# Kernel optimization log

Measured on AMD Instinct MI355X. Metric: run time of the kernel, lower is better.

The kernel has to match this reference:

```python
import jax, jax.numpy as jnp
import numpy as np

DIM = 128
N_NODES = 100000
N_EDGES = 640000


def setup_inputs() -> dict:
    key = jax.random.key(0)
    k1, k2, k3, k4, k5, k6 = jax.random.split(key, 6)
    x = jax.random.normal(k1, (N_NODES, DIM), dtype=jnp.float32)
    edge_index = jax.random.randint(k2, (2, N_EDGES), 0, N_NODES, dtype=jnp.int64)
    edge_weight = jax.random.uniform(k3, (N_EDGES,), dtype=jnp.float32)
    # Linear(dim, dim) params (PyTorch stores weight as [out, in])
    bound = 1.0 / np.sqrt(DIM)
    W = jax.random.uniform(k4, (DIM, DIM), minval=-bound, maxval=bound, dtype=jnp.float32)
    b = jax.random.uniform(k5, (DIM,), minval=-bound, maxval=bound, dtype=jnp.float32)
    alpha = jnp.float32(0.5)
    return {"x": x, "edge_index": edge_index, "num_nodes": N_NODES,
            "edge_weight": edge_weight, "W": W, "b": b, "alpha": alpha}


def reference(x, edge_index, num_nodes, edge_weight, W, b, alpha):
    src = edge_index[0]
    dst = edge_index[1]
    msg = x[src] * edge_weight[:, None]                      # [E, D] gather + weight
    agg = jax.ops.segment_sum(msg, dst, num_segments=num_nodes)   # [N, D] scatter-add
    deg = jax.ops.segment_sum(jnp.ones_like(edge_weight), dst, num_segments=num_nodes)
    deg = jnp.maximum(deg, 1.0)                              # clamp(min=1.0)
    agg = agg / deg[:, None]                                 # mean normalization
    return x + alpha * (agg @ W.T + b)                       # linear + alpha residual
```

## Files before the change

### kernel.cpp

```cpp
#include <hip/hip_runtime.h>
#include <hip/hip_bf16.h>

#define DIM 128
#define NPB 512
#define NPB_SHIFT 9

#define A1_EPT 8
#define A1_EPB (256 * A1_EPT)
#define NBLK_STRIDE 512

#define FROWS 64
#define FPAD 136

typedef __attribute__((ext_vector_type(8))) short bf16x8;
typedef __attribute__((ext_vector_type(8))) unsigned short u16x8;
typedef __attribute__((ext_vector_type(4))) float f32x4;

__device__ __forceinline__ short f2bf(float f) {
    union { __hip_bfloat16 h; short s; } u;
    u.h = __float2bfloat16(f);
    return u.s;
}
__device__ __forceinline__ float bf2f(unsigned short s) {
    union { unsigned int u; float f; } c;
    c.u = ((unsigned int)s) << 16;
    return c.f;
}

__device__ __forceinline__ int load_dst(const void* eidx, int flag64, int E, int e) {
    return flag64 ? (int)((const long long*)eidx)[E + e] : ((const int*)eidx)[E + e];
}
__device__ __forceinline__ int load_src(const void* eidx, int flag64, int E, int e) {
    return flag64 ? (int)((const long long*)eidx)[e] : ((const int*)eidx)[e];
}

__global__ __launch_bounds__(256) void prep_kernel(
        const float* __restrict__ x, unsigned short* __restrict__ xb, int n8,
        const unsigned int* __restrict__ e, int* __restrict__ flags) {
    const int stride = gridDim.x * blockDim.x;
    const int t0 = blockIdx.x * blockDim.x + threadIdx.x;
    for (int t = t0; t < n8; t += stride) {
        const float4* pp = (const float4*)(x + (size_t)t * 8);
        float4 a = pp[0], b = pp[1];
        u16x8 o;
        o[0] = (unsigned short)f2bf(a.x); o[1] = (unsigned short)f2bf(a.y);
        o[2] = (unsigned short)f2bf(a.z); o[3] = (unsigned short)f2bf(a.w);
        o[4] = (unsigned short)f2bf(b.x); o[5] = (unsigned short)f2bf(b.y);
        o[6] = (unsigned short)f2bf(b.z); o[7] = (unsigned short)f2bf(b.w);
        *(u16x8*)(xb + (size_t)t * 8) = o;
    }
    if (blockIdx.x == 0 && threadIdx.x == 0) {
        int ok64 = 1;
        for (int t = 0; t < 128; ++t) {
            if (e[2 * t + 1] != 0u) { ok64 = 0; break; }
        }
        flags[0] = ok64;
    }
}

__global__ __launch_bounds__(256) void part1_kernel(
        const void* __restrict__ eidx, int* __restrict__ bhistT,
        const int* __restrict__ flags, int E) {
    __shared__ int bcnt[256];
    const int tid = threadIdx.x;
    const int blk = blockIdx.x;
    const int base = blk * A1_EPB;
    const int f = flags[0];
    bcnt[tid] = 0;
    __syncthreads();
    #pragma unroll
    for (int i = 0; i < A1_EPT; ++i) {
        int e = base + tid + i * 256;
        if (e < E) atomicAdd(&bcnt[load_dst(eidx, f, E, e) >> NPB_SHIFT], 1);
    }
    __syncthreads();
    bhistT[tid * NBLK_STRIDE + blk] = bcnt[tid];
}

__global__ __launch_bounds__(512) void scancol_kernel(
        int* __restrict__ bhistT, int* __restrict__ colsum, int nblk) {
    __shared__ int s[512];
    const int tid = threadIdx.x;
    const int bu = blockIdx.x;
    int v = (tid < nblk) ? bhistT[bu * NBLK_STRIDE + tid] : 0;
    s[tid] = v;
    __syncthreads();
    for (int off = 1; off < 512; off <<= 1) {
        int t = (tid >= off) ? s[tid - off] : 0;
        __syncthreads();
        s[tid] += t;
        __syncthreads();
    }
    if (tid < nblk) bhistT[bu * NBLK_STRIDE + tid] = s[tid] - v;
    if (tid == 511) colsum[bu] = s[511];
}

__global__ __launch_bounds__(256) void scanb_kernel(
        const int* __restrict__ colsum, int* __restrict__ gstart, int NB, int E) {
    __shared__ int s[256];
    const int tid = threadIdx.x;
    int val = (tid < NB) ? colsum[tid] : 0;
    s[tid] = val;
    __syncthreads();
    for (int off = 1; off < 256; off <<= 1) {
        int t = (tid >= off) ? s[tid - off] : 0;
        __syncthreads();
        s[tid] += t;
        __syncthreads();
    }
    if (tid < NB) gstart[tid] = s[tid] - val;
    if (tid == NB) gstart[NB] = E;
}

__global__ __launch_bounds__(256) void part2_kernel(
        const void* __restrict__ eidx, const float* __restrict__ ew,
        const int* __restrict__ bhistT, const int* __restrict__ gstart,
        unsigned long long* __restrict__ srcw_tmp,
        const int* __restrict__ flags, int E) {
    __shared__ unsigned long long stage[A1_EPB];
    __shared__ unsigned char sbid[A1_EPB];
    __shared__ int bcnt[256], bscan[256], bcur[256], brun[256];
    const int tid = threadIdx.x;
    const int blk = blockIdx.x;
    const int base = blk * A1_EPB;
    const int f = flags[0];

    bcnt[tid] = 0;
    __syncthreads();

    unsigned long long pk[A1_EPT];
    unsigned char bid[A1_EPT];
    #pragma unroll
    for (int i = 0; i < A1_EPT; ++i) {
        int e = base + tid + i * 256;
        bid[i] = 0xFF;
        if (e < E) {
            int src = load_src(eidx, f, E, e);
            int dst = load_dst(eidx, f, E, e);
            unsigned int w = __float_as_uint(ew[e]);
            int b = dst >> NPB_SHIFT;
            pk[i] = ((unsigned long long)w << 26)
                  | ((unsigned long long)(dst & (NPB - 1)) << 17)
                  | (unsigned long long)(unsigned)src;
            bid[i] = (unsigned char)b;
            atomicAdd(&bcnt[b], 1);
        }
    }
    __syncthreads();

    int val = bcnt[tid];
    bscan[tid] = val;
    __syncthreads();
    for (int off = 1; off < 256; off <<= 1) {
        int t = (tid >= off) ? bscan[tid - off] : 0;
        __syncthreads();
        bscan[tid] += t;
        __syncthreads();
    }
    int excl = bscan[tid] - val;
    __syncthreads();
    bscan[tid] = excl;
    bcur[tid] = excl;
    brun[tid] = gstart[tid] + bhistT[tid * NBLK_STRIDE + blk];
    __syncthreads();

    #pragma unroll
    for (int i = 0; i < A1_EPT; ++i) {
        if (bid[i] != 0xFF) {
            int slot = atomicAdd(&bcur[bid[i]], 1);
            stage[slot] = pk[i];
            sbid[slot] = bid[i];
        }
    }
    __syncthreads();

    int tot = (base + A1_EPB <= E) ? A1_EPB : (E - base);
    for (int s = tid; s < tot; s += 256) {
        int b = sbid[s];
        srcw_tmp[brun[b] + (s - bscan[b])] = stage[s];
    }
}

__global__ __launch_bounds__(512) void sort_kernel(
        const unsigned long long* __restrict__ srcw_tmp,
        const int* __restrict__ gstart, unsigned long long* __restrict__ srcw,
        int* __restrict__ rowstart, int nn) {
    __shared__ int cnt[NPB], cur[NPB], s[NPB];
    const int tid = threadIdx.x;
    const int b = blockIdx.x;
    const int node0 = b << NPB_SHIFT;
    const int e0 = gstart[b], e1 = gstart[b + 1];

    cnt[tid] = 0;
    __syncthreads();
    for (int e = e0 + tid; e < e1; e += 512)
        atomicAdd(&cnt[(int)((srcw_tmp[e] >> 17) & (NPB - 1))], 1);
    __syncthreads();

    int val = cnt[tid];
    s[tid] = val;
    __syncthreads();
    for (int off = 1; off < 512; off <<= 1) {
        int t = (tid >= off) ? s[tid - off] : 0;
        __syncthreads();
        s[tid] += t;
        __syncthreads();
    }
    int excl = s[tid] - val;
    cur[tid] = excl;
    __syncthreads();

    int nbn = nn - node0; if (nbn > NPB) nbn = NPB;
    if (tid < nbn) rowstart[node0 + tid] = e0 + excl;

    for (int e = e0 + tid; e < e1; e += 512) {
        unsigned long long pk = srcw_tmp[e];
        int dl = (int)((pk >> 17) & (NPB - 1));
        int pos = e0 + atomicAdd(&cur[dl], 1);
        srcw[pos] = ((pk >> 26) << 32) | (pk & 0x1FFFFULL);
    }
}

__global__ __launch_bounds__(256) void gather_kernel(
        const unsigned short* __restrict__ xb, const uint2* __restrict__ srcw,
        const int* __restrict__ rowstart, unsigned short* __restrict__ aggb,
        int nn, int E) {
    int g = (blockIdx.x * blockDim.x + threadIdx.x) >> 4;
    int sub16 = threadIdx.x & 15;
    if (g >= nn) return;
    int n0 = rowstart[g];
    int n1 = (g + 1 < nn) ? rowstart[g + 1] : E;
    float acc[8] = {0.f, 0.f, 0.f, 0.f, 0.f, 0.f, 0.f, 0.f};
    int e = n0;
    for (; e + 4 <= n1; e += 4) {
        uint2 sw0 = srcw[e];
        uint2 sw1 = srcw[e + 1];
        uint2 sw2 = srcw[e + 2];
        uint2 sw3 = srcw[e + 3];
        u16x8 x0 = *(const u16x8*)(xb + (size_t)sw0.x * DIM + sub16 * 8);
        u16x8 x1 = *(const u16x8*)(xb + (size_t)sw1.x * DIM + sub16 * 8);
        u16x8 x2 = *(const u16x8*)(xb + (size_t)sw2.x * DIM + sub16 * 8);
        u16x8 x3 = *(const u16x8*)(xb + (size_t)sw3.x * DIM + sub16 * 8);
        float w0 = __uint_as_float(sw0.y);
        float w1 = __uint_as_float(sw1.y);
        float w2 = __uint_as_float(sw2.y);
        float w3 = __uint_as_float(sw3.y);
        #pragma unroll
        for (int j = 0; j < 8; ++j) {
            acc[j] = fmaf(bf2f(x0[j]), w0, acc[j]);
            acc[j] = fmaf(bf2f(x1[j]), w1, acc[j]);
            acc[j] = fmaf(bf2f(x2[j]), w2, acc[j]);
            acc[j] = fmaf(bf2f(x3[j]), w3, acc[j]);
        }
    }
    for (; e < n1; ++e) {
        uint2 sw = srcw[e];
        u16x8 xr = *(const u16x8*)(xb + (size_t)sw.x * DIM + sub16 * 8);
        float w = __uint_as_float(sw.y);
        #pragma unroll
        for (int j = 0; j < 8; ++j) acc[j] = fmaf(bf2f(xr[j]), w, acc[j]);
    }
    float inv = 1.0f / fmaxf((float)(n1 - n0), 1.0f);
    u16x8 o;
    #pragma unroll
    for (int j = 0; j < 8; ++j) o[j] = (unsigned short)f2bf(acc[j] * inv);
    *(u16x8*)(aggb + (size_t)g * DIM + sub16 * 8) = o;
}

__global__ __launch_bounds__(512) void finish_kernel(
        const unsigned short* __restrict__ aggb, float* __restrict__ out,
        const unsigned short* __restrict__ xb, const float* __restrict__ W,
        const float* __restrict__ bias, const float* __restrict__ alphaP, int nn) {
    __shared__ alignas(16) unsigned short A_lds[FROWS * FPAD];
    const int tid  = threadIdx.x;
    const int wv   = tid >> 6;
    const int lane = tid & 63;
    const int half = lane >> 4;
    const int l16  = lane & 15;
    const int b0   = blockIdx.x * FROWS;
    const float alpha = alphaP[0];

    const int jcol = wv * 16 + l16;
    bf16x8 bfrag[4];
    #pragma unroll
    for (int kt = 0; kt < 4; ++kt) {
        const float4* w4 = (const float4*)(W + (size_t)jcol * DIM + kt * 32 + half * 8);
        float4 lo = w4[0], hi = w4[1];
        bf16x8 b;
        b[0] = f2bf(lo.x); b[1] = f2bf(lo.y); b[2] = f2bf(lo.z); b[3] = f2bf(lo.w);
        b[4] = f2bf(hi.x); b[5] = f2bf(hi.y); b[6] = f2bf(hi.z); b[7] = f2bf(hi.w);
        bfrag[kt] = b;
    }
    const float bias_j = bias[jcol];

    #pragma unroll
    for (int it = 0; it < 2; ++it) {
        int p = it * 512 + tid;
        int row = p >> 4;
        int c8 = p & 15;
        int node = b0 + row;
        u16x8 v = {0, 0, 0, 0, 0, 0, 0, 0};
        if (node < nn) v = *(const u16x8*)(aggb + (size_t)node * DIM + c8 * 8);
        *(u16x8*)&A_lds[row * FPAD + c8 * 8] = v;
    }
    __syncthreads();

    #pragma unroll
    for (int mt = 0; mt < 4; ++mt) {
        f32x4 acc = {0.f, 0.f, 0.f, 0.f};
        #pragma unroll
        for (int kt = 0; kt < 4; ++kt) {
            const bf16x8 a = *(const bf16x8*)&A_lds[(mt * 16 + l16) * FPAD + kt * 32 + half * 8];
            acc = __builtin_amdgcn_mfma_f32_16x16x32_bf16(a, bfrag[kt], acc, 0, 0, 0);
        }
        #pragma unroll
        for (int r = 0; r < 4; ++r) {
            int grow = b0 + mt * 16 + half * 4 + r;
            if (grow < nn) {
                size_t idx = (size_t)grow * DIM + jcol;
                out[idx] = bf2f(xb[idx]) + alpha * (acc[r] + bias_j);
            }
        }
    }
}

extern "C" void kernel_launch(void* const* d_in, const int* in_sizes, int n_in,
                              void* d_out, int out_size, void* d_ws, size_t ws_size,
                              hipStream_t stream) {
    const float* x      = (const float*)d_in[0];
    const void*  eidx   = d_in[1];
    const float* ew     = (const float*)d_in[3];
    const float* W      = (const float*)d_in[4];
    const float* bias   = (const float*)d_in[5];
    const float* alphaP = (const float*)d_in[6];

    const int NN = in_sizes[0] / DIM;
    const int E  = in_sizes[3];
    const int NB = (NN + NPB - 1) / NPB;
    const int nblk = (E + A1_EPB - 1) / A1_EPB;

    unsigned short* aggb = (unsigned short*)d_ws;
    unsigned short* xb   = aggb + (size_t)NN * DIM;
    unsigned long long* srcw     = (unsigned long long*)(xb + (size_t)NN * DIM);
    unsigned long long* srcw_tmp = srcw + E;
    int* rowstart = (int*)(srcw_tmp + E);
    int* bhistT   = rowstart + NN;
    int* colsum   = bhistT + 256 * NBLK_STRIDE;
    int* gstart   = colsum + 256;
    int* flags    = gstart + 257;

    float* out = (float*)d_out;

    int n8 = NN * DIM / 8;
    prep_kernel<<<2048, 256, 0, stream>>>(x, xb, n8, (const unsigned int*)eidx, flags);

    part1_kernel<<<nblk, 256, 0, stream>>>(eidx, bhistT, flags, E);

    scancol_kernel<<<NB, 512, 0, stream>>>(bhistT, colsum, nblk);

    scanb_kernel<<<1, 256, 0, stream>>>(colsum, gstart, NB, E);

    part2_kernel<<<nblk, 256, 0, stream>>>(eidx, ew, bhistT, gstart, srcw_tmp, flags, E);

    sort_kernel<<<NB, 512, 0, stream>>>(srcw_tmp, gstart, srcw, rowstart, NN);

    int gblocks = (NN + 15) / 16;
    gather_kernel<<<gblocks, 256, 0, stream>>>(xb, (const uint2*)srcw, rowstart,
                                               aggb, NN, E);

    int fblocks = (NN + FROWS - 1) / FROWS;
    finish_kernel<<<fblocks, 512, 0, stream>>>(aggb, out, xb, W, bias, alphaP, NN);
}
```

Baseline: 102.4 us.

## Fuse dst histogram into bf16 prep kernel and widen gather batching to eight edges

The separate part1 histogram kernel is folded into prep_kernel: its first nblk blocks compute the per-block destination-bucket counts alongside the x-to-bf16 conversion, and each block detects the 64-bit index format locally instead of reading a global flag. This removes one kernel launch and the flag dependency between launches. Separately, the gather loop now issues eight srcw/xb loads per iteration with masked padding (padding entries read row 0 with zero weight) instead of four plus a scalar tail, which raises memory-level parallelism but adds wasted loads for low-degree nodes and more registers. Each part2 block also repeats the 128-word detection scan serially on one thread.

```diff
diff --git a/kernel.cpp b/kernel.cpp
--- a/kernel.cpp
+++ b/kernel.cpp
@@ -34,12 +34,42 @@
     return flag64 ? (int)((const long long*)eidx)[e] : ((const int*)eidx)[e];
 }
 
+__device__ __forceinline__ int detect64_block(const unsigned int* e, int* sdet) {
+    if (threadIdx.x == 0) {
+        int ok64 = 1;
+        for (int t = 0; t < 128; ++t) {
+            if (e[2 * t + 1] != 0u) { ok64 = 0; break; }
+        }
+        *sdet = ok64;
+    }
+    __syncthreads();
+    return *sdet;
+}
+
 __global__ __launch_bounds__(256) void prep_kernel(
         const float* __restrict__ x, unsigned short* __restrict__ xb, int n8,
-        const unsigned int* __restrict__ e, int* __restrict__ flags) {
+        const void* __restrict__ eidx, int* __restrict__ bhistT, int E, int nblk) {
+    __shared__ int bcnt[256];
+    __shared__ int sdet;
+    const int tid = threadIdx.x;
+    const int blk = blockIdx.x;
+    const bool hist = (blk < nblk);
+
+    int f = 0;
+    if (hist) {
+        f = detect64_block((const unsigned int*)eidx, &sdet);
+        bcnt[tid] = 0;
+        __syncthreads();
+        const int base = blk * A1_EPB;
+        #pragma unroll
+        for (int i = 0; i < A1_EPT; ++i) {
+            int e = base + tid + i * 256;
+            if (e < E) atomicAdd(&bcnt[load_dst(eidx, f, E, e) >> NPB_SHIFT], 1);
+        }
+    }
+
     const int stride = gridDim.x * blockDim.x;
-    const int t0 = blockIdx.x * blockDim.x + threadIdx.x;
-    for (int t = t0; t < n8; t += stride) {
+    for (int t = blk * blockDim.x + tid; t < n8; t += stride) {
         const float4* pp = (const float4*)(x + (size_t)t * 8);
         float4 a = pp[0], b = pp[1];
         u16x8 o;
@@ -49,32 +79,11 @@
         o[6] = (unsigned short)f2bf(b.z); o[7] = (unsigned short)f2bf(b.w);
         *(u16x8*)(xb + (size_t)t * 8) = o;
     }
-    if (blockIdx.x == 0 && threadIdx.x == 0) {
-        int ok64 = 1;
-        for (int t = 0; t < 128; ++t) {
-            if (e[2 * t + 1] != 0u) { ok64 = 0; break; }
-        }
-        flags[0] = ok64;
-    }
-}
-
-__global__ __launch_bounds__(256) void part1_kernel(
-        const void* __restrict__ eidx, int* __restrict__ bhistT,
-        const int* __restrict__ flags, int E) {
-    __shared__ int bcnt[256];
-    const int tid = threadIdx.x;
-    const int blk = blockIdx.x;
-    const int base = blk * A1_EPB;
-    const int f = flags[0];
-    bcnt[tid] = 0;
-    __syncthreads();
-    #pragma unroll
-    for (int i = 0; i < A1_EPT; ++i) {
-        int e = base + tid + i * 256;
-        if (e < E) atomicAdd(&bcnt[load_dst(eidx, f, E, e) >> NPB_SHIFT], 1);
-    }
-    __syncthreads();
-    bhistT[tid * NBLK_STRIDE + blk] = bcnt[tid];
+
+    if (hist) {
+        __syncthreads();
+        bhistT[tid * NBLK_STRIDE + blk] = bcnt[tid];
+    }
 }
 
 __global__ __launch_bounds__(512) void scancol_kernel(
@@ -115,15 +124,15 @@
 __global__ __launch_bounds__(256) void part2_kernel(
         const void* __restrict__ eidx, const float* __restrict__ ew,
         const int* __restrict__ bhistT, const int* __restrict__ gstart,
-        unsigned long long* __restrict__ srcw_tmp,
-        const int* __restrict__ flags, int E) {
+        unsigned long long* __restrict__ srcw_tmp, int E) {
     __shared__ unsigned long long stage[A1_EPB];
     __shared__ unsigned char sbid[A1_EPB];
     __shared__ int bcnt[256], bscan[256], bcur[256], brun[256];
+    __shared__ int sdet;
     const int tid = threadIdx.x;
     const int blk = blockIdx.x;
     const int base = blk * A1_EPB;
-    const int f = flags[0];
+    const int f = detect64_block((const unsigned int*)eidx, &sdet);
 
     bcnt[tid] = 0;
     __syncthreads();
@@ -231,34 +240,25 @@
     int n0 = rowstart[g];
     int n1 = (g + 1 < nn) ? rowstart[g + 1] : E;
     float acc[8] = {0.f, 0.f, 0.f, 0.f, 0.f, 0.f, 0.f, 0.f};
-    int e = n0;
-    for (; e + 4 <= n1; e += 4) {
-        uint2 sw0 = srcw[e];
-        uint2 sw1 = srcw[e + 1];
-        uint2 sw2 = srcw[e + 2];
-        uint2 sw3 = srcw[e + 3];
-        u16x8 x0 = *(const u16x8*)(xb + (size_t)sw0.x * DIM + sub16 * 8);
-        u16x8 x1 = *(const u16x8*)(xb + (size_t)sw1.x * DIM + sub16 * 8);
-        u16x8 x2 = *(const u16x8*)(xb + (size_t)sw2.x * DIM + sub16 * 8);
-        u16x8 x3 = *(const u16x8*)(xb + (size_t)sw3.x * DIM + sub16 * 8);
-        float w0 = __uint_as_float(sw0.y);
-        float w1 = __uint_as_float(sw1.y);
-        float w2 = __uint_as_float(sw2.y);
-        float w3 = __uint_as_float(sw3.y);
-        #pragma unroll
-        for (int j = 0; j < 8; ++j) {
-            acc[j] = fmaf(bf2f(x0[j]), w0, acc[j]);
-            acc[j] = fmaf(bf2f(x1[j]), w1, acc[j]);
-            acc[j] = fmaf(bf2f(x2[j]), w2, acc[j]);
-            acc[j] = fmaf(bf2f(x3[j]), w3, acc[j]);
-        }
-    }
-    for (; e < n1; ++e) {
-        uint2 sw = srcw[e];
-        u16x8 xr = *(const u16x8*)(xb + (size_t)sw.x * DIM + sub16 * 8);
-        float w = __uint_as_float(sw.y);
-        #pragma unroll
-        for (int j = 0; j < 8; ++j) acc[j] = fmaf(bf2f(xr[j]), w, acc[j]);
+    for (int e = n0; e < n1; e += 8) {
+        int rem = n1 - e;
+        uint2 sws[8];
+        #pragma unroll
+        for (int i = 0; i < 8; ++i) {
+            if (i < rem) sws[i] = srcw[e + i];
+            else { sws[i].x = 0u; sws[i].y = 0u; }
+        }
+        u16x8 xs[8];
+        #pragma unroll
+        for (int i = 0; i < 8; ++i)
+            xs[i] = *(const u16x8*)(xb + (size_t)sws[i].x * DIM + sub16 * 8);
+        #pragma unroll
+        for (int i = 0; i < 8; ++i) {
+            float w = __uint_as_float(sws[i].y);
+            #pragma unroll
+            for (int j = 0; j < 8; ++j)
+                acc[j] = fmaf(bf2f(xs[i][j]), w, acc[j]);
+        }
     }
     float inv = 1.0f / fmaxf((float)(n1 - n0), 1.0f);
     u16x8 o;
@@ -347,20 +347,17 @@
     int* bhistT   = rowstart + NN;
     int* colsum   = bhistT + 256 * NBLK_STRIDE;
     int* gstart   = colsum + 256;
-    int* flags    = gstart + 257;
 
     float* out = (float*)d_out;
 
     int n8 = NN * DIM / 8;
-    prep_kernel<<<2048, 256, 0, stream>>>(x, xb, n8, (const unsigned int*)eidx, flags);
-
-    part1_kernel<<<nblk, 256, 0, stream>>>(eidx, bhistT, flags, E);
+    prep_kernel<<<2048, 256, 0, stream>>>(x, xb, n8, eidx, bhistT, E, nblk);
 
     scancol_kernel<<<NB, 512, 0, stream>>>(bhistT, colsum, nblk);
 
     scanb_kernel<<<1, 256, 0, stream>>>(colsum, gstart, NB, E);
 
-    part2_kernel<<<nblk, 256, 0, stream>>>(eidx, ew, bhistT, gstart, srcw_tmp, flags, E);
+    part2_kernel<<<nblk, 256, 0, stream>>>(eidx, ew, bhistT, gstart, srcw_tmp, E);
 
     sort_kernel<<<NB, 512, 0, stream>>>(srcw_tmp, gstart, srcw, rowstart, NN);
 
```

After: 101.9 us (median of 2 runs). Within noise of the previous version (-0.5%).
